# Performance work log

Measured on AMD Instinct MI355X. Metric: run time of the kernel, lower is better.

The kernel has to match this reference:

```python
import jax, jax.numpy as jnp
import numpy as np

N_NODES = 100000
N_EDGES = 3200000
N_GRAPHS = 256
IN_CH = 8
HID = 64
N_REL = 2


def rgcn_conv(x, edge_index, edge_type, W, root, bias):
    # W: [R, in, out]; PyG RGCNConv with aggr='mean' per relation, summed across relations
    n = x.shape[0]
    src, dst = edge_index[0], edge_index[1]
    H = jnp.einsum('ni,rio->rno', x, W)                      # [R, N, out]
    msgs = H[edge_type, src]                                  # [E, out]
    # per-(node, relation) in-degree for the mean
    seg = dst * N_REL + edge_type
    deg = jax.ops.segment_sum(jnp.ones_like(edge_type, dtype=x.dtype), seg,
                              num_segments=n * N_REL)
    norm = jnp.maximum(deg[seg], 1.0)
    agg = jax.ops.segment_sum(msgs / norm[:, None], dst, num_segments=n)  # [N, out]
    return agg + x @ root + bias


def setup_inputs() -> dict:
    key = jax.random.key(0)
    ks = jax.random.split(key, 16)
    x = jax.random.normal(ks[0], (N_NODES, IN_CH), dtype=jnp.float32)
    edge_index = jax.random.randint(ks[1], (2, N_EDGES), 0, N_NODES, dtype=jnp.int64)
    edge_type = jax.random.randint(ks[2], (N_EDGES,), 0, N_REL, dtype=jnp.int64)
    batch = jnp.sort(jax.random.randint(ks[3], (N_NODES,), 0, N_GRAPHS, dtype=jnp.int64))

    def glorot(k, shape):
        fan_in, fan_out = shape[-2], shape[-1]
        s = float(np.sqrt(6.0 / (fan_in + fan_out)))
        return jax.random.uniform(k, shape, dtype=jnp.float32, minval=-s, maxval=s)

    params = {
        'W1': glorot(ks[4], (N_REL, IN_CH, HID)), 'root1': glorot(ks[5], (IN_CH, HID)),
        'b1': jnp.zeros((HID,), jnp.float32),
        'W2': glorot(ks[6], (N_REL, HID, HID)), 'root2': glorot(ks[7], (HID, HID)),
        'b2': jnp.zeros((HID,), jnp.float32),
        'W3': glorot(ks[8], (N_REL, HID, HID)), 'root3': glorot(ks[9], (HID, HID)),
        'b3': jnp.zeros((HID,), jnp.float32),
        'cW1': glorot(ks[10], (HID, HID // 2)), 'cb1': jnp.zeros((HID // 2,), jnp.float32),
        'cW2': glorot(ks[11], (HID // 2, 1)), 'cb2': jnp.zeros((1,), jnp.float32),
    }
    return {'x': x, 'edge_index': edge_index, 'edge_type': edge_type, 'batch': batch, **params}


def reference(x, edge_index, edge_type, batch,
              W1, root1, b1, W2, root2, b2, W3, root3, b3,
              cW1, cb1, cW2, cb2):
    h = jax.nn.relu(rgcn_conv(x, edge_index, edge_type, W1, root1, b1))
    h = jax.nn.relu(rgcn_conv(h, edge_index, edge_type, W2, root2, b2))
    h = rgcn_conv(h, edge_index, edge_type, W3, root3, b3)
    g = jax.ops.segment_sum(h, batch, num_segments=N_GRAPHS)   # global_add_pool
    # dropout is identity in eval mode
    g = jax.nn.relu(g @ cW1 + cb1)
    return g @ cW2 + cb2                                        # [N_GRAPHS, 1]
```

## Files before the change

kernel.cpp:

```cpp
#include <hip/hip_runtime.h>


typedef unsigned int uint;
typedef unsigned short ushort;
typedef __attribute__((ext_vector_type(8))) short bf16x8;
typedef __attribute__((ext_vector_type(4))) float f32x4;
typedef __attribute__((ext_vector_type(2))) float f32x2;

#define EPB 6144
#define BCAP 8960

__device__ __forceinline__ uint bf1(float f){
  uint u = __float_as_uint(f);
  return (u + 0x7fffu + ((u>>16)&1u)) >> 16;
}
__device__ __forceinline__ uint bfpack2(float lo, float hi){
  return bf1(lo) | (bf1(hi)<<16);
}
__device__ __forceinline__ f32x2 cvt2lo(uint w){
  f32x2 r; r.x = __uint_as_float(w<<16); r.y = __uint_as_float(w & 0xffff0000u);
  return r;
}
__device__ __forceinline__ void red2(f32x2& a){
  a.x += __shfl_xor(a.x,16); a.x += __shfl_xor(a.x,32);
  a.y += __shfl_xor(a.y,16); a.y += __shfl_xor(a.y,32);
}
__device__ __forceinline__ void acc2(uint2 w, float sg,
    f32x2& tL, f32x2& tH, f32x2& dL, f32x2& dH){
  f32x2 lo = cvt2lo(w.x), hi = cvt2lo(w.y);
  f32x2 s2 = {sg, sg};
  tL += lo; tH += hi;
  dL += s2*lo; dH += s2*hi;
}

__global__ __launch_bounds__(1024) void k_part(const int* __restrict__ ei,
    const int* __restrict__ et, int* __restrict__ bcur,
    uint* __restrict__ bk, int E, int NBK){
  __shared__ uint   stg[EPB];
  __shared__ ushort stgb[EPB];
  __shared__ int h[400];
  __shared__ int basep[400];
  __shared__ int loc[400];
  __shared__ int tot_s;
  int t = threadIdx.x;
  int base = blockIdx.x*EPB;

  int e0=base+t,      e1=base+t+1024, e2=base+t+2048;
  int e3=base+t+3072, e4=base+t+4096, e5=base+t+5120;
  bool v0=e0<E, v1=e1<E, v2=e2<E, v3=e3<E, v4=e4<E, v5=e5<E;
  int s0=0,d0=0,y0=0,s1=0,d1=0,y1=0,s2=0,d2=0,y2=0;
  int s3=0,d3=0,y3=0,s4=0,d4=0,y4=0,s5=0,d5=0,y5=0;
  if (v0){ s0=ei[e0]; d0=ei[E+e0]; y0=et[e0]; }
  if (v1){ s1=ei[e1]; d1=ei[E+e1]; y1=et[e1]; }
  if (v2){ s2=ei[e2]; d2=ei[E+e2]; y2=et[e2]; }
  if (v3){ s3=ei[e3]; d3=ei[E+e3]; y3=et[e3]; }
  if (v4){ s4=ei[e4]; d4=ei[E+e4]; y4=et[e4]; }
  if (v5){ s5=ei[e5]; d5=ei[E+e5]; y5=et[e5]; }

  for (int i=t;i<NBK;i+=1024) h[i]=0;
  __syncthreads();
  int r0=0,r1=0,r2=0,r3=0,r4=0,r5=0;
  if (v0) r0 = atomicAdd(&h[d0>>8], 1);
  if (v1) r1 = atomicAdd(&h[d1>>8], 1);
  if (v2) r2 = atomicAdd(&h[d2>>8], 1);
  if (v3) r3 = atomicAdd(&h[d3>>8], 1);
  if (v4) r4 = atomicAdd(&h[d4>>8], 1);
  if (v5) r5 = atomicAdd(&h[d5>>8], 1);
  __syncthreads();
  if (t < 64){
    int pre[8]; int s = 0;
    #pragma unroll
    for (int j=0;j<8;++j){
      int idx = t*8+j;
      int c = (idx < NBK) ? h[idx] : 0;
      pre[j] = s; s += c;
    }
    int run = s;
    #pragma unroll
    for (int off=1; off<64; off<<=1){
      int u = __shfl_up(run, off);
      if (t >= off) run += u;
    }
    int excl = run - s;
    #pragma unroll
    for (int j=0;j<8;++j){
      int idx = t*8+j;
      if (idx < NBK) loc[idx] = excl + pre[j];
    }
    if (t == 63) tot_s = run;
  } else if (t >= 64 && t < 64 + NBK){
    int bu = t - 64;
    int c = h[bu];
    basep[bu] = c ? (bu*BCAP + atomicAdd(&bcur[bu], c)) : 0;
  }
  __syncthreads();
  if (v0){ int bu=d0>>8, p=loc[bu]+r0; stg[p]=((uint)s0<<9)|(uint)(((d0&255)<<1)|y0); stgb[p]=(ushort)bu; }
  if (v1){ int bu=d1>>8, p=loc[bu]+r1; stg[p]=((uint)s1<<9)|(uint)(((d1&255)<<1)|y1); stgb[p]=(ushort)bu; }
  if (v2){ int bu=d2>>8, p=loc[bu]+r2; stg[p]=((uint)s2<<9)|(uint)(((d2&255)<<1)|y2); stgb[p]=(ushort)bu; }
  if (v3){ int bu=d3>>8, p=loc[bu]+r3; stg[p]=((uint)s3<<9)|(uint)(((d3&255)<<1)|y3); stgb[p]=(ushort)bu; }
  if (v4){ int bu=d4>>8, p=loc[bu]+r4; stg[p]=((uint)s4<<9)|(uint)(((d4&255)<<1)|y4); stgb[p]=(ushort)bu; }
  if (v5){ int bu=d5>>8, p=loc[bu]+r5; stg[p]=((uint)s5<<9)|(uint)(((d5&255)<<1)|y5); stgb[p]=(ushort)bu; }
  __syncthreads();
  int tot = tot_s;
  for (int i=t; i<tot; i+=1024){
    int bu  = stgb[i];
    int abs_ = basep[bu] + (i - loc[bu]);
    if (abs_ < (bu+1)*BCAP) bk[abs_] = stg[i];
  }
}

__global__ __launch_bounds__(1024) void k_csr(const uint* __restrict__ bk,
    const int* __restrict__ bcur, int* __restrict__ deg,
    int* __restrict__ pos, int* __restrict__ ssrc, int N,
    const float* __restrict__ W2, const float* __restrict__ root2,
    const float* __restrict__ W3, const float* __restrict__ root3,
    ushort* __restrict__ wt2, ushort* __restrict__ wt3,
    float* __restrict__ gp, ushort* __restrict__ h1z,
    ushort* __restrict__ h2z, int NBK, int G){
  __shared__ uint stg[BCAP];
  __shared__ int h[512];
  __shared__ int cur[512];
  int b = blockIdx.x, t = threadIdx.x;
  if (b >= NBK){
    const float* Wl = (b==NBK) ? W2 : W3;
    const float* rp = (b==NBK) ? root2 : root3;
    ushort* wt = (b==NBK) ? wt2 : wt3;
    for (int i=t; i<64*192; i+=1024){
      int n = i/192, k = i - n*192;
      float v = (k<128) ? Wl[k*64+n] : rp[(k-128)*64+n];
      wt[i] = (ushort)bf1(v);
    }
    if (b==NBK+1){
      for (int i=t;i<G*64;i+=1024) gp[i]=0.f;
      if (t < 64){
        h1z[(size_t)N*64 + t] = 0;
        h2z[(size_t)N*64 + t] = 0;
      }
    }
    return;
  }
  int start = b*BCAP;
  int cnt = bcur[b]; if (cnt > BCAP) cnt = BCAP;
  if (t < 512) h[t]=0;
  for (int i=t; i<cnt; i+=1024) stg[i] = bk[start+i];
  __syncthreads();
  for (int i=t; i<cnt; i+=1024) atomicAdd(&h[stg[i]&511], 1);
  __syncthreads();
  if (t < 64){
    int c0v[4], c1v[4], pre[4]; int s = 0;
    #pragma unroll
    for (int j=0;j<4;++j){
      int idx = t*4+j;
      c0v[j] = h[2*idx]; c1v[j] = h[2*idx+1];
      pre[j] = s; s += c0v[j] + c1v[j];
    }
    int run = s;
    #pragma unroll
    for (int off=1; off<64; off<<=1){
      int u = __shfl_up(run, off);
      if (t >= off) run += u;
    }
    int excl = run - s;
    #pragma unroll
    for (int j=0;j<4;++j){
      int idx = t*4+j;
      int base0 = start + excl + pre[j];
      cur[2*idx]   = base0;
      cur[2*idx+1] = base0 + c0v[j];
      int node = (b<<8) + idx;
      if (node < N){
        deg[(b<<9)+2*idx]   = c0v[j]; deg[(b<<9)+2*idx+1] = c1v[j];
        pos[(b<<9)+2*idx]   = base0;  pos[(b<<9)+2*idx+1] = base0 + c0v[j];
      }
    }
  }
  __syncthreads();
  for (int i=t; i<cnt; i+=1024){
    uint w = stg[i];
    int p = atomicAdd(&cur[w & 511], 1);
    ssrc[p] = (int)(w >> 9);
  }
}

__global__ __launch_bounds__(256) void k_gather64(
    const ushort* __restrict__ hp, const int* __restrict__ deg,
    const int* __restrict__ pos, const int* __restrict__ ssrc,
    ushort* __restrict__ sn, int N)
{
  int lane = threadIdx.x & 63;
  int wid  = (blockIdx.x*256 + threadIdx.x) >> 6;
  int c4 = lane & 15, eg = lane >> 4;
  int nA = wid*2, nB = nA+1;
  if (nA >= N) return;
  int d0A = __builtin_amdgcn_readfirstlane(deg[2*nA]);
  int d1A = __builtin_amdgcn_readfirstlane(deg[2*nA+1]);
  int pA  = __builtin_amdgcn_readfirstlane(pos[2*nA]);
  int cA  = d0A + d1A;
  int d0B = 0, d1B = 0, pB = 0, cB = 0;
  if (nB < N){
    d0B = __builtin_amdgcn_readfirstlane(deg[2*nB]);
    d1B = __builtin_amdgcn_readfirstlane(deg[2*nB+1]);
    pB  = __builtin_amdgcn_readfirstlane(pos[2*nB]);
    cB  = d0B+d1B;
  }

  f32x2 totAL={0,0}, totAH={0,0}, difAL={0,0}, difAH={0,0};
  f32x2 totBL={0,0}, totBH={0,0}, difBL={0,0}, difBH={0,0};
  int jA = 0, jB = 0;
  while (jA < cA || jB < cB){
    int tA = cA - jA; if (tA > 64) tA = 64;
    int tB = cB - jB; if (tB > 64) tB = 64;
    int r0A = d0A - jA, r0B = d0B - jB;
    int svA = N, svB = N;
    if (lane < tA) svA = ssrc[pA + jA + lane];
    if (lane < tB) svB = ssrc[pB + jB + lane];
    float ssA = (lane < r0A) ? 1.f : -1.f;
    float ssB = (lane < r0B) ? 1.f : -1.f;
    int mt = tA > tB ? tA : tB;
    for (int e = 0; e < mt; e += 8){
      int i0 = e + eg, i1 = e + 4 + eg;
      int a0 = __shfl(svA, i0), b0 = __shfl(svB, i0);
      int a1 = __shfl(svA, i1), b1 = __shfl(svB, i1);
      float sA0 = __shfl(ssA, i0), sB0 = __shfl(ssB, i0);
      float sA1 = __shfl(ssA, i1), sB1 = __shfl(ssB, i1);
      uint2 wA0 = *(const uint2*)(hp + (size_t)a0*64 + c4*4);
      uint2 wB0 = *(const uint2*)(hp + (size_t)b0*64 + c4*4);
      uint2 wA1 = *(const uint2*)(hp + (size_t)a1*64 + c4*4);
      uint2 wB1 = *(const uint2*)(hp + (size_t)b1*64 + c4*4);
      acc2(wA0, sA0, totAL, totAH, difAL, difAH);
      acc2(wB0, sB0, totBL, totBH, difBL, difBH);
      acc2(wA1, sA1, totAL, totAH, difAL, difAH);
      acc2(wB1, sB1, totBL, totBH, difBL, difBH);
    }
    jA += tA; jB += tB;
  }
  red2(totAL); red2(totAH); red2(difAL); red2(difAH);
  red2(totBL); red2(totBH); red2(difBL); red2(difBH);
  int rel = (lane >> 4) & 1;
  float4 tt_, dd_;
  if (lane < 32){
    tt_ = make_float4(totAL.x, totAL.y, totAH.x, totAH.y);
    dd_ = make_float4(difAL.x, difAL.y, difAH.x, difAH.y);
  } else {
    tt_ = make_float4(totBL.x, totBL.y, totBH.x, totBH.y);
    dd_ = make_float4(difBL.x, difBL.y, difBH.x, difBH.y);
  }
  int dsel = (lane < 32) ? (rel ? d1A : d0A) : (rel ? d1B : d0B);
  float sg = rel ? -1.f : 1.f;
  float id = 0.5f / (float)(dsel > 1 ? dsel : 1);
  float4 v;
  v.x = fmaf(sg, dd_.x, tt_.x) * id;
  v.y = fmaf(sg, dd_.y, tt_.y) * id;
  v.z = fmaf(sg, dd_.z, tt_.z) * id;
  v.w = fmaf(sg, dd_.w, tt_.w) * id;
  int n = (lane < 32) ? nA : nB;
  if (n < N){
    uint2 pkt; pkt.x = bfpack2(v.x, v.y); pkt.y = bfpack2(v.z, v.w);
    *(uint2*)(sn + (size_t)n*128 + rel*64 + c4*4) = pkt;
  }
}

__global__ __launch_bounds__(256) void k_l1(
    const float* __restrict__ xp, const int* __restrict__ deg,
    const int* __restrict__ pos, const int* __restrict__ ssrc,
    const float* __restrict__ W1,
    const float* __restrict__ root1,
    const float* __restrict__ b1,
    ushort* __restrict__ h1, int N)
{
  int lane = threadIdx.x & 63;
  int wid  = (blockIdx.x*256 + threadIdx.x) >> 6;
  int c = lane & 7, eg = lane >> 3;
  int nA = wid*2, nB = nA+1;
  if (nA >= N) return;
  int d0A = __builtin_amdgcn_readfirstlane(deg[2*nA]);
  int d1A = __builtin_amdgcn_readfirstlane(deg[2*nA+1]);
  int pA  = __builtin_amdgcn_readfirstlane(pos[2*nA]);
  int cA  = d0A + d1A;
  int d0B = 0, d1B = 0, pB = 0, cB = 0;
  if (nB < N){
    d0B = __builtin_amdgcn_readfirstlane(deg[2*nB]);
    d1B = __builtin_amdgcn_readfirstlane(deg[2*nB+1]);
    pB  = __builtin_amdgcn_readfirstlane(pos[2*nB]);
    cB  = d0B+d1B;
  }

  float totA=0.f, s1A=0.f, totB=0.f, s1B=0.f;
  int jA = 0, jB = 0;
  while (jA < cA || jB < cB){
    int tA = cA - jA; if (tA > 64) tA = 64;
    int tB = cB - jB; if (tB > 64) tB = 64;
    int svA = (lane < tA) ? ssrc[pA + jA + lane] : 0;
    int svB = (lane < tB) ? ssrc[pB + jB + lane] : 0;
    int mt = tA > tB ? tA : tB;
    for (int e = 0; e < mt; e += 32){
      int i0 = e + eg, i1 = e + 8 + eg, i2 = e + 16 + eg, i3 = e + 24 + eg;
      int a0 = __shfl(svA, i0), a1 = __shfl(svA, i1);
      int a2 = __shfl(svA, i2), a3 = __shfl(svA, i3);
      int b0 = __shfl(svB, i0), b1 = __shfl(svB, i1);
      int b2 = __shfl(svB, i2), b3 = __shfl(svB, i3);
      float vA0 = xp[(size_t)a0*8 + c];
      float vA1 = xp[(size_t)a1*8 + c];
      float vA2 = xp[(size_t)a2*8 + c];
      float vA3 = xp[(size_t)a3*8 + c];
      float vB0 = xp[(size_t)b0*8 + c];
      float vB1 = xp[(size_t)b1*8 + c];
      float vB2 = xp[(size_t)b2*8 + c];
      float vB3 = xp[(size_t)b3*8 + c];
      vA0 = (i0 < tA) ? vA0 : 0.f;
      vA1 = (i1 < tA) ? vA1 : 0.f;
      vA2 = (i2 < tA) ? vA2 : 0.f;
      vA3 = (i3 < tA) ? vA3 : 0.f;
      vB0 = (i0 < tB) ? vB0 : 0.f;
      vB1 = (i1 < tB) ? vB1 : 0.f;
      vB2 = (i2 < tB) ? vB2 : 0.f;
      vB3 = (i3 < tB) ? vB3 : 0.f;
      totA += vA0;  s1A += ((jA + i0) >= d0A) ? vA0 : 0.f;
      totA += vA1;  s1A += ((jA + i1) >= d0A) ? vA1 : 0.f;
      totA += vA2;  s1A += ((jA + i2) >= d0A) ? vA2 : 0.f;
      totA += vA3;  s1A += ((jA + i3) >= d0A) ? vA3 : 0.f;
      totB += vB0;  s1B += ((jB + i0) >= d0B) ? vB0 : 0.f;
      totB += vB1;  s1B += ((jB + i1) >= d0B) ? vB1 : 0.f;
      totB += vB2;  s1B += ((jB + i2) >= d0B) ? vB2 : 0.f;
      totB += vB3;  s1B += ((jB + i3) >= d0B) ? vB3 : 0.f;
    }
    jA += tA; jB += tB;
  }
  float s0A = totA - s1A, s0B = totB - s1B;
  #pragma unroll
  for (int off=8; off<64; off<<=1){
    s0A += __shfl_xor(s0A, off); s1A += __shfl_xor(s1A, off);
    s0B += __shfl_xor(s0B, off); s1B += __shfl_xor(s1B, off);
  }
  s0A *= 1.f/(float)(d0A>1?d0A:1);  s1A *= 1.f/(float)(d1A>1?d1A:1);
  s0B *= 1.f/(float)(d0B>1?d0B:1);  s1B *= 1.f/(float)(d1B>1?d1B:1);

  int ch = lane;
  float accA = b1[ch], accB = accA;
  #pragma unroll
  for (int k = 0; k < 8; ++k){
    float wv = W1[k*64 + ch];
    accA = fmaf(__shfl(s0A, k), wv, accA);
    accB = fmaf(__shfl(s0B, k), wv, accB);
  }
  #pragma unroll
  for (int k = 0; k < 8; ++k){
    float wv = W1[512 + k*64 + ch];
    accA = fmaf(__shfl(s1A, k), wv, accA);
    accB = fmaf(__shfl(s1B, k), wv, accB);
  }
  #pragma unroll
  for (int k = 0; k < 8; ++k){
    float wr = root1[k*64 + ch];
    float xa = xp[(size_t)nA*8 + k];
    accA = fmaf(xa, wr, accA);
    if (nB < N){
      float xb = xp[(size_t)nB*8 + k];
      accB = fmaf(xb, wr, accB);
    }
  }
  accA = fmaxf(accA, 0.f);
  h1[(size_t)nA*64 + ch] = (ushort)bf1(accA);
  if (nB < N){
    accB = fmaxf(accB, 0.f);
    h1[(size_t)nB*64 + ch] = (ushort)bf1(accB);
  }
}

template<int RELU, int OUTBF>
__global__ __launch_bounds__(256) void k_mm192m(
    const ushort* __restrict__ sn,
    const ushort* __restrict__ hp,
    const ushort* __restrict__ wt,
    const float* __restrict__ bias, void* __restrict__ hout_, int N)
{
  int t = threadIdx.x, lane = t & 63, w = t >> 6;
  int quad = lane >> 4, l15 = lane & 15;
  int nb = blockIdx.x * 64;
  int node = nb + w*16 + l15;
  int ncl = node < N ? node : N-1;
  const ushort* arow_sn = sn + (size_t)ncl*128 + quad*8;
  const ushort* arow_hp = hp + (size_t)ncl*64  + quad*8;

  f32x4 acc0={0,0,0,0}, acc1={0,0,0,0}, acc2_={0,0,0,0}, acc3={0,0,0,0};
  #pragma unroll
  for (int ks = 0; ks < 6; ++ks){
    bf16x8 a = (ks < 4) ? *(const bf16x8*)(arow_sn + ks*32)
                        : *(const bf16x8*)(arow_hp + (ks-4)*32);
    const ushort* wk = wt + (size_t)l15*192 + ks*32 + quad*8;
    bf16x8 b0 = *(const bf16x8*)(wk);
    bf16x8 b1 = *(const bf16x8*)(wk + 16*192);
    bf16x8 b2 = *(const bf16x8*)(wk + 32*192);
    bf16x8 b3 = *(const bf16x8*)(wk + 48*192);
    acc0 = __builtin_amdgcn_mfma_f32_16x16x32_bf16(a, b0, acc0, 0,0,0);
    acc1 = __builtin_amdgcn_mfma_f32_16x16x32_bf16(a, b1, acc1, 0,0,0);
    acc2_ = __builtin_amdgcn_mfma_f32_16x16x32_bf16(a, b2, acc2_, 0,0,0);
    acc3 = __builtin_amdgcn_mfma_f32_16x16x32_bf16(a, b3, acc3, 0,0,0);
  }
  f32x4 accs[4] = {acc0, acc1, acc2_, acc3};
  #pragma unroll
  for (int tt = 0; tt < 4; ++tt){
    int n = tt*16 + l15;
    float bv = bias[n];
    #pragma unroll
    for (int i = 0; i < 4; ++i){
      int nd = nb + w*16 + quad*4 + i;
      if (nd < N){
        float v = accs[tt][i] + bv;
        if (RELU) v = fmaxf(v, 0.f);
        if (OUTBF) ((ushort*)hout_)[(size_t)nd*64 + n] = (ushort)bf1(v);
        else       ((float*)hout_)[(size_t)nd*64 + n] = v;
      }
    }
  }
}

__global__ __launch_bounds__(256) void k_mm192pool(
    const ushort* __restrict__ sn, const ushort* __restrict__ hp,
    const ushort* __restrict__ wt, const float* __restrict__ bias,
    const int* __restrict__ batch, float* __restrict__ gp, int N)
{
  __shared__ float hl[64*66];
  __shared__ int bl[64];
  int t = threadIdx.x, lane = t & 63, w = t >> 6;
  int quad = lane >> 4, l15 = lane & 15;
  int nb = blockIdx.x * 64;
  int node = nb + w*16 + l15;
  int ncl = node < N ? node : N-1;
  const ushort* arow_sn = sn + (size_t)ncl*128 + quad*8;
  const ushort* arow_hp = hp + (size_t)ncl*64  + quad*8;

  f32x4 acc0={0,0,0,0}, acc1={0,0,0,0}, acc2_={0,0,0,0}, acc3={0,0,0,0};
  #pragma unroll
  for (int ks = 0; ks < 6; ++ks){
    bf16x8 a = (ks < 4) ? *(const bf16x8*)(arow_sn + ks*32)
                        : *(const bf16x8*)(arow_hp + (ks-4)*32);
    const ushort* wk = wt + (size_t)l15*192 + ks*32 + quad*8;
    bf16x8 b0 = *(const bf16x8*)(wk);
    bf16x8 b1 = *(const bf16x8*)(wk + 16*192);
    bf16x8 b2 = *(const bf16x8*)(wk + 32*192);
    bf16x8 b3 = *(const bf16x8*)(wk + 48*192);
    acc0 = __builtin_amdgcn_mfma_f32_16x16x32_bf16(a, b0, acc0, 0,0,0);
    acc1 = __builtin_amdgcn_mfma_f32_16x16x32_bf16(a, b1, acc1, 0,0,0);
    acc2_ = __builtin_amdgcn_mfma_f32_16x16x32_bf16(a, b2, acc2_, 0,0,0);
    acc3 = __builtin_amdgcn_mfma_f32_16x16x32_bf16(a, b3, acc3, 0,0,0);
  }
  f32x4 accs[4] = {acc0, acc1, acc2_, acc3};
  #pragma unroll
  for (int tt = 0; tt < 4; ++tt){
    int ch = tt*16 + l15;
    float bv = bias[ch];
    #pragma unroll
    for (int i = 0; i < 4; ++i){
      int nl = w*16 + quad*4 + i;
      hl[nl*66 + ch] = accs[tt][i] + bv;
    }
  }
  if (t < 64) bl[t] = (nb + t < N) ? batch[nb + t] : -1;
  __syncthreads();
  int c = t & 63, q = t >> 6;
  float acc = 0.f; int curg = -1;
  #pragma unroll 4
  for (int i = 0; i < 16; ++i){
    int nl = q*16 + i;
    int g = bl[nl];
    if (g != curg){
      if (curg >= 0) atomicAdd(&gp[curg*64 + c], acc);
      curg = g; acc = 0.f;
    }
    if (g >= 0) acc += hl[nl*66 + c];
  }
  if (curg >= 0) atomicAdd(&gp[curg*64 + c], acc);
}

__global__ __launch_bounds__(256) void k_clf(const float* __restrict__ gp,
    const float* __restrict__ cW1, const float* __restrict__ cb1,
    const float* __restrict__ cW2, const float* __restrict__ cb2,
    float* __restrict__ out, int G){
  int lane = threadIdx.x & 63;
  int g = (blockIdx.x*256 + threadIdx.x) >> 6;
  if (g >= G) return;
  int j = lane & 31, half = lane >> 5;
  const float* gv = gp + (size_t)g*64 + half*32;
  const float* Wc = cW1 + half*32*32 + j;
  float s = 0.f;
  #pragma unroll 8
  for (int i=0;i<32;++i) s += gv[i] * Wc[i*32];
  s += __shfl_xor(s, 32);
  s = fmaxf(s + cb1[j], 0.f) * cW2[j];
  s += __shfl_xor(s, 1);  s += __shfl_xor(s, 2);
  s += __shfl_xor(s, 4);  s += __shfl_xor(s, 8);
  s += __shfl_xor(s, 16);
  if (lane == 0) out[g] = s + cb2[0];
}

extern "C" void kernel_launch(void* const* d_in, const int* in_sizes, int n_in,
                              void* d_out, int out_size, void* d_ws, size_t ws_size,
                              hipStream_t stream){
  const float* x     = (const float*)d_in[0];
  const int*   ei    = (const int*)d_in[1];
  const int*   et    = (const int*)d_in[2];
  const int*   batch = (const int*)d_in[3];
  const float* W1    = (const float*)d_in[4];
  const float* root1 = (const float*)d_in[5];
  const float* b1    = (const float*)d_in[6];
  const float* W2    = (const float*)d_in[7];
  const float* root2 = (const float*)d_in[8];
  const float* b2    = (const float*)d_in[9];
  const float* W3    = (const float*)d_in[10];
  const float* root3 = (const float*)d_in[11];
  const float* b3    = (const float*)d_in[12];
  const float* cW1   = (const float*)d_in[13];
  const float* cb1   = (const float*)d_in[14];
  const float* cW2   = (const float*)d_in[15];
  const float* cb2   = (const float*)d_in[16];
  float* out = (float*)d_out;
  (void)n_in; (void)ws_size;

  int N = in_sizes[0]/8;
  int E = in_sizes[2];
  int G = out_size;
  int M = 2*N;
  int NBK = (N + 255) >> 8;

  char* w = (char*)d_ws;
  auto alloc=[&](size_t bytes)->char*{ char* p=w; w += (bytes+255)&~(size_t)255; return p; };
  int*    bcur  = (int*)alloc(1024*4);
  int*    ssrc  = (int*)alloc((size_t)NBK*BCAP*4);
  int*    deg   = (int*)alloc((size_t)M*4);
  int*    pos   = (int*)alloc((size_t)M*4);
  ushort* h1    = (ushort*)alloc((size_t)(N+1)*64*2);
  ushort* snU   = (ushort*)alloc((size_t)N*128*2);
  ushort* h2    = (ushort*)alloc((size_t)(N+1)*64*2);
  float*  gp    = (float*)alloc((size_t)G*64*4);
  ushort* wt2   = (ushort*)alloc(64*192*2);
  ushort* wt3   = (ushort*)alloc(64*192*2);
  uint*   bk    = (uint*)snU;

  hipMemsetAsync(bcur, 0, (size_t)NBK*4, stream);
  int nbE = (E + EPB - 1)/EPB;
  k_part <<<nbE,1024,0,stream>>>(ei,et,bcur,bk,E,NBK);
  k_csr  <<<NBK+2,1024,0,stream>>>(bk,bcur,deg,pos,ssrc,N,
                                   W2,root2,W3,root3,wt2,wt3,gp,h1,h2,NBK,G);

  int gb = (((N+1)/2) + 3) / 4;
  int nbk = (N+63)/64;
  k_l1<<<gb,256,0,stream>>>(x,deg,pos,ssrc,W1,root1,b1,h1,N);
  k_gather64<<<gb,256,0,stream>>>(h1,deg,pos,ssrc,snU,N);
  k_mm192m<1,1><<<nbk,256,0,stream>>>(snU,h1,wt2,b2,h2,N);
  k_gather64<<<gb,256,0,stream>>>(h2,deg,pos,ssrc,snU,N);
  k_mm192pool<<<nbk,256,0,stream>>>(snU,h2,wt3,b3,batch,gp,N);
  k_clf<<<(G*64+255)/256,256,0,stream>>>(gp,cW1,cb1,cW2,cb2,out,G);
}
```

Measured before the change: 351.0 us.

## Fuse layer-1 aggregation into CSR build kernel using shared degree/offset data

```diff
diff --git a/kernel.cpp b/kernel.cpp
--- a/kernel.cpp
+++ b/kernel.cpp
@@ -115,11 +115,15 @@
     const float* __restrict__ W2, const float* __restrict__ root2,
     const float* __restrict__ W3, const float* __restrict__ root3,
     ushort* __restrict__ wt2, ushort* __restrict__ wt3,
-    float* __restrict__ gp, ushort* __restrict__ h1z,
-    ushort* __restrict__ h2z, int NBK, int G){
+    float* __restrict__ gp, ushort* __restrict__ h1,
+    ushort* __restrict__ h2z,
+    const float* __restrict__ xp, const float* __restrict__ W1,
+    const float* __restrict__ root1, const float* __restrict__ b1,
+    int NBK, int G){
   __shared__ uint stg[BCAP];
   __shared__ int h[512];
   __shared__ int cur[512];
+  __shared__ int pstart[512];
   int b = blockIdx.x, t = threadIdx.x;
   if (b >= NBK){
     const float* Wl = (b==NBK) ? W2 : W3;
@@ -133,7 +137,7 @@
     if (b==NBK+1){
       for (int i=t;i<G*64;i+=1024) gp[i]=0.f;
       if (t < 64){
-        h1z[(size_t)N*64 + t] = 0;
+        h1[(size_t)N*64 + t] = 0;
         h2z[(size_t)N*64 + t] = 0;
       }
     }
@@ -165,8 +169,10 @@
     for (int j=0;j<4;++j){
       int idx = t*4+j;
       int base0 = start + excl + pre[j];
-      cur[2*idx]   = base0;
-      cur[2*idx+1] = base0 + c0v[j];
+      cur[2*idx]    = base0;
+      cur[2*idx+1]  = base0 + c0v[j];
+      pstart[2*idx]   = base0;
+      pstart[2*idx+1] = base0 + c0v[j];
       int node = (b<<8) + idx;
       if (node < N){
         deg[(b<<9)+2*idx]   = c0v[j]; deg[(b<<9)+2*idx+1] = c1v[j];
@@ -179,6 +185,102 @@
     uint w = stg[i];
     int p = atomicAdd(&cur[w & 511], 1);
     ssrc[p] = (int)(w >> 9);
+  }
+  __syncthreads();
+
+  int lane = t & 63, w = t >> 6;
+  int c = lane & 7, eg = lane >> 3;
+  for (int r = 0; r < 8; ++r){
+    int i2 = w*16 + r*2;
+    int nA = (b<<8) + i2, nB = nA + 1;
+    int d0A = __builtin_amdgcn_readfirstlane(h[2*i2]);
+    int d1A = __builtin_amdgcn_readfirstlane(h[2*i2+1]);
+    int pA  = __builtin_amdgcn_readfirstlane(pstart[2*i2]);
+    int d0B = __builtin_amdgcn_readfirstlane(h[2*i2+2]);
+    int d1B = __builtin_amdgcn_readfirstlane(h[2*i2+3]);
+    int pB  = __builtin_amdgcn_readfirstlane(pstart[2*i2+2]);
+    if (nA >= N){ d0A = 0; d1A = 0; }
+    if (nB >= N){ d0B = 0; d1B = 0; }
+    int cA = d0A + d1A, cB = d0B + d1B;
+
+    float totA=0.f, s1A=0.f, totB=0.f, s1B=0.f;
+    int jA = 0, jB = 0;
+    while (jA < cA || jB < cB){
+      int tA = cA - jA; if (tA > 64) tA = 64;
+      int tB = cB - jB; if (tB > 64) tB = 64;
+      int svA = (lane < tA) ? ssrc[pA + jA + lane] : 0;
+      int svB = (lane < tB) ? ssrc[pB + jB + lane] : 0;
+      int mt = tA > tB ? tA : tB;
+      for (int e = 0; e < mt; e += 32){
+        int i0 = e + eg, i1 = e + 8 + eg, i2_ = e + 16 + eg, i3 = e + 24 + eg;
+        int a0 = __shfl(svA, i0), a1 = __shfl(svA, i1);
+        int a2 = __shfl(svA, i2_), a3 = __shfl(svA, i3);
+        int b0 = __shfl(svB, i0), b1 = __shfl(svB, i1);
+        int b2 = __shfl(svB, i2_), b3 = __shfl(svB, i3);
+        float vA0 = xp[(size_t)a0*8 + c];
+        float vA1 = xp[(size_t)a1*8 + c];
+        float vA2 = xp[(size_t)a2*8 + c];
+        float vA3 = xp[(size_t)a3*8 + c];
+        float vB0 = xp[(size_t)b0*8 + c];
+        float vB1 = xp[(size_t)b1*8 + c];
+        float vB2 = xp[(size_t)b2*8 + c];
+        float vB3 = xp[(size_t)b3*8 + c];
+        vA0 = (i0 < tA) ? vA0 : 0.f;
+        vA1 = (i1 < tA) ? vA1 : 0.f;
+        vA2 = (i2_ < tA) ? vA2 : 0.f;
+        vA3 = (i3 < tA) ? vA3 : 0.f;
+        vB0 = (i0 < tB) ? vB0 : 0.f;
+        vB1 = (i1 < tB) ? vB1 : 0.f;
+        vB2 = (i2_ < tB) ? vB2 : 0.f;
+        vB3 = (i3 < tB) ? vB3 : 0.f;
+        totA += vA0;  s1A += ((jA + i0) >= d0A) ? vA0 : 0.f;
+        totA += vA1;  s1A += ((jA + i1) >= d0A) ? vA1 : 0.f;
+        totA += vA2;  s1A += ((jA + i2_) >= d0A) ? vA2 : 0.f;
+        totA += vA3;  s1A += ((jA + i3) >= d0A) ? vA3 : 0.f;
+        totB += vB0;  s1B += ((jB + i0) >= d0B) ? vB0 : 0.f;
+        totB += vB1;  s1B += ((jB + i1) >= d0B) ? vB1 : 0.f;
+        totB += vB2;  s1B += ((jB + i2_) >= d0B) ? vB2 : 0.f;
+        totB += vB3;  s1B += ((jB + i3) >= d0B) ? vB3 : 0.f;
+      }
+      jA += tA; jB += tB;
+    }
+    float s0A = totA - s1A, s0B = totB - s1B;
+    #pragma unroll
+    for (int off=8; off<64; off<<=1){
+      s0A += __shfl_xor(s0A, off); s1A += __shfl_xor(s1A, off);
+      s0B += __shfl_xor(s0B, off); s1B += __shfl_xor(s1B, off);
+    }
+    s0A *= 1.f/(float)(d0A>1?d0A:1);  s1A *= 1.f/(float)(d1A>1?d1A:1);
+    s0B *= 1.f/(float)(d0B>1?d0B:1);  s1B *= 1.f/(float)(d1B>1?d1B:1);
+
+    int ch = lane;
+    float accA = b1[ch], accB = accA;
+    #pragma unroll
+    for (int k = 0; k < 8; ++k){
+      float wv = W1[k*64 + ch];
+      accA = fmaf(__shfl(s0A, k), wv, accA);
+      accB = fmaf(__shfl(s0B, k), wv, accB);
+    }
+    #pragma unroll
+    for (int k = 0; k < 8; ++k){
+      float wv = W1[512 + k*64 + ch];
+      accA = fmaf(__shfl(s1A, k), wv, accA);
+      accB = fmaf(__shfl(s1B, k), wv, accB);
+    }
+    if (nA < N){
+      float acc = accA;
+      #pragma unroll
+      for (int k = 0; k < 8; ++k)
+        acc = fmaf(xp[(size_t)nA*8 + k], root1[k*64 + ch], acc);
+      h1[(size_t)nA*64 + ch] = (ushort)bf1(fmaxf(acc, 0.f));
+    }
+    if (nB < N){
+      float acc = accB;
+      #pragma unroll
+      for (int k = 0; k < 8; ++k)
+        acc = fmaf(xp[(size_t)nB*8 + k], root1[k*64 + ch], acc);
+      h1[(size_t)nB*64 + ch] = (ushort)bf1(fmaxf(acc, 0.f));
+    }
   }
 }
 
@@ -260,113 +362,6 @@
   }
 }
 
-__global__ __launch_bounds__(256) void k_l1(
-    const float* __restrict__ xp, const int* __restrict__ deg,
-    const int* __restrict__ pos, const int* __restrict__ ssrc,
-    const float* __restrict__ W1,
-    const float* __restrict__ root1,
-    const float* __restrict__ b1,
-    ushort* __restrict__ h1, int N)
-{
-  int lane = threadIdx.x & 63;
-  int wid  = (blockIdx.x*256 + threadIdx.x) >> 6;
-  int c = lane & 7, eg = lane >> 3;
-  int nA = wid*2, nB = nA+1;
-  if (nA >= N) return;
-  int d0A = __builtin_amdgcn_readfirstlane(deg[2*nA]);
-  int d1A = __builtin_amdgcn_readfirstlane(deg[2*nA+1]);
-  int pA  = __builtin_amdgcn_readfirstlane(pos[2*nA]);
-  int cA  = d0A + d1A;
-  int d0B = 0, d1B = 0, pB = 0, cB = 0;
-  if (nB < N){
-    d0B = __builtin_amdgcn_readfirstlane(deg[2*nB]);
-    d1B = __builtin_amdgcn_readfirstlane(deg[2*nB+1]);
-    pB  = __builtin_amdgcn_readfirstlane(pos[2*nB]);
-    cB  = d0B+d1B;
-  }
-
-  float totA=0.f, s1A=0.f, totB=0.f, s1B=0.f;
-  int jA = 0, jB = 0;
-  while (jA < cA || jB < cB){
-    int tA = cA - jA; if (tA > 64) tA = 64;
-    int tB = cB - jB; if (tB > 64) tB = 64;
-    int svA = (lane < tA) ? ssrc[pA + jA + lane] : 0;
-    int svB = (lane < tB) ? ssrc[pB + jB + lane] : 0;
-    int mt = tA > tB ? tA : tB;
-    for (int e = 0; e < mt; e += 32){
-      int i0 = e + eg, i1 = e + 8 + eg, i2 = e + 16 + eg, i3 = e + 24 + eg;
-      int a0 = __shfl(svA, i0), a1 = __shfl(svA, i1);
-      int a2 = __shfl(svA, i2), a3 = __shfl(svA, i3);
-      int b0 = __shfl(svB, i0), b1 = __shfl(svB, i1);
-      int b2 = __shfl(svB, i2), b3 = __shfl(svB, i3);
-      float vA0 = xp[(size_t)a0*8 + c];
-      float vA1 = xp[(size_t)a1*8 + c];
-      float vA2 = xp[(size_t)a2*8 + c];
-      float vA3 = xp[(size_t)a3*8 + c];
-      float vB0 = xp[(size_t)b0*8 + c];
-      float vB1 = xp[(size_t)b1*8 + c];
-      float vB2 = xp[(size_t)b2*8 + c];
-      float vB3 = xp[(size_t)b3*8 + c];
-      vA0 = (i0 < tA) ? vA0 : 0.f;
-      vA1 = (i1 < tA) ? vA1 : 0.f;
-      vA2 = (i2 < tA) ? vA2 : 0.f;
-      vA3 = (i3 < tA) ? vA3 : 0.f;
-      vB0 = (i0 < tB) ? vB0 : 0.f;
-      vB1 = (i1 < tB) ? vB1 : 0.f;
-      vB2 = (i2 < tB) ? vB2 : 0.f;
-      vB3 = (i3 < tB) ? vB3 : 0.f;
-      totA += vA0;  s1A += ((jA + i0) >= d0A) ? vA0 : 0.f;
-      totA += vA1;  s1A += ((jA + i1) >= d0A) ? vA1 : 0.f;
-      totA += vA2;  s1A += ((jA + i2) >= d0A) ? vA2 : 0.f;
-      totA += vA3;  s1A += ((jA + i3) >= d0A) ? vA3 : 0.f;
-      totB += vB0;  s1B += ((jB + i0) >= d0B) ? vB0 : 0.f;
-      totB += vB1;  s1B += ((jB + i1) >= d0B) ? vB1 : 0.f;
-      totB += vB2;  s1B += ((jB + i2) >= d0B) ? vB2 : 0.f;
-      totB += vB3;  s1B += ((jB + i3) >= d0B) ? vB3 : 0.f;
-    }
-    jA += tA; jB += tB;
-  }
-  float s0A = totA - s1A, s0B = totB - s1B;
-  #pragma unroll
-  for (int off=8; off<64; off<<=1){
-    s0A += __shfl_xor(s0A, off); s1A += __shfl_xor(s1A, off);
-    s0B += __shfl_xor(s0B, off); s1B += __shfl_xor(s1B, off);
-  }
-  s0A *= 1.f/(float)(d0A>1?d0A:1);  s1A *= 1.f/(float)(d1A>1?d1A:1);
-  s0B *= 1.f/(float)(d0B>1?d0B:1);  s1B *= 1.f/(float)(d1B>1?d1B:1);
-
-  int ch = lane;
-  float accA = b1[ch], accB = accA;
-  #pragma unroll
-  for (int k = 0; k < 8; ++k){
-    float wv = W1[k*64 + ch];
-    accA = fmaf(__shfl(s0A, k), wv, accA);
-    accB = fmaf(__shfl(s0B, k), wv, accB);
-  }
-  #pragma unroll
-  for (int k = 0; k < 8; ++k){
-    float wv = W1[512 + k*64 + ch];
-    accA = fmaf(__shfl(s1A, k), wv, accA);
-    accB = fmaf(__shfl(s1B, k), wv, accB);
-  }
-  #pragma unroll
-  for (int k = 0; k < 8; ++k){
-    float wr = root1[k*64 + ch];
-    float xa = xp[(size_t)nA*8 + k];
-    accA = fmaf(xa, wr, accA);
-    if (nB < N){
-      float xb = xp[(size_t)nB*8 + k];
-      accB = fmaf(xb, wr, accB);
-    }
-  }
-  accA = fmaxf(accA, 0.f);
-  h1[(size_t)nA*64 + ch] = (ushort)bf1(accA);
-  if (nB < N){
-    accB = fmaxf(accB, 0.f);
-    h1[(size_t)nB*64 + ch] = (ushort)bf1(accB);
-  }
-}
-
 template<int RELU, int OUTBF>
 __global__ __launch_bounds__(256) void k_mm192m(
     const ushort* __restrict__ sn,
@@ -541,11 +536,11 @@
   int nbE = (E + EPB - 1)/EPB;
   k_part <<<nbE,1024,0,stream>>>(ei,et,bcur,bk,E,NBK);
   k_csr  <<<NBK+2,1024,0,stream>>>(bk,bcur,deg,pos,ssrc,N,
-                                   W2,root2,W3,root3,wt2,wt3,gp,h1,h2,NBK,G);
+                                   W2,root2,W3,root3,wt2,wt3,gp,h1,h2,
+                                   x,W1,root1,b1,NBK,G);
 
   int gb = (((N+1)/2) + 3) / 4;
   int nbk = (N+63)/64;
-  k_l1<<<gb,256,0,stream>>>(x,deg,pos,ssrc,W1,root1,b1,h1,N);
   k_gather64<<<gb,256,0,stream>>>(h1,deg,pos,ssrc,snU,N);
   k_mm192m<1,1><<<nbk,256,0,stream>>>(snU,h1,wt2,b2,h2,N);
   k_gather64<<<gb,256,0,stream>>>(h2,deg,pos,ssrc,snU,N);
```

After: 362.0 us. 3.2% more time.
